# Kernel tuning notes

Hardware: AMD Instinct MI355X
Metric: run time of the kernel (lower is better)

## Reference

```python
import jax, jax.numpy as jnp
import numpy as np

GROUPS = 32
EPS = 1e-5


def group_norm(x, gamma, beta):
    B, C, D, H, W = x.shape
    xr = x.reshape(B, GROUPS, C // GROUPS, D, H, W)
    mean = xr.mean(axis=(2, 3, 4, 5), keepdims=True)
    var = xr.var(axis=(2, 3, 4, 5), keepdims=True)
    xn = (xr - mean) * jax.lax.rsqrt(var + EPS)
    xn = xn.reshape(B, C, D, H, W)
    return xn * gamma[None, :, None, None, None] + beta[None, :, None, None, None]


def conv1x1(h, w, b):
    # 1x1x1 Conv3d == channel matmul. w: [O, C], b: [O]
    return jnp.einsum('oc,bcdhw->bodhw', w, h) + b[None, :, None, None, None]


def setup_inputs() -> dict:
    key = jax.random.key(0)
    ks = jax.random.split(key, 10)
    B, C, D, H, W = 2, 128, 16, 16, 16
    x = jax.random.normal(ks[0], (B, C, D, H, W), dtype=jnp.float32)
    gn_w = jnp.ones((C,), dtype=jnp.float32)
    gn_b = jnp.zeros((C,), dtype=jnp.float32)
    # xavier_uniform for [C, C, 1, 1, 1] conv: fan_in = fan_out = C
    lim = float(np.sqrt(6.0 / (C + C)))
    wq = jax.random.uniform(ks[1], (C, C), jnp.float32, -lim, lim)
    wk = jax.random.uniform(ks[2], (C, C), jnp.float32, -lim, lim)
    wv = jax.random.uniform(ks[3], (C, C), jnp.float32, -lim, lim)
    wp = jax.random.uniform(ks[4], (C, C), jnp.float32, -lim, lim) * 1e-05
    bq = jnp.zeros((C,), jnp.float32)
    bk = jnp.zeros((C,), jnp.float32)
    bv = jnp.zeros((C,), jnp.float32)
    bp = jnp.zeros((C,), jnp.float32)
    return {"x": x, "gn_w": gn_w, "gn_b": gn_b, "wq": wq, "bq": bq,
            "wk": wk, "bk": bk, "wv": wv, "bv": bv, "wp": wp, "bp": bp}


def reference(x, gn_w, gn_b, wq, bq, wk, bk, wv, bv, wp, bp):
    B, C, D, H, W = x.shape
    N = D * H * W
    h = group_norm(x, gn_w, gn_b)
    q = conv1x1(h, wq, bq)
    k = conv1x1(h, wk, bk)
    v = conv1x1(h, wv, bv)
    q = q.transpose(0, 2, 3, 4, 1).reshape(B, N, C)   # [B, N, C]
    k = k.reshape(B, C, N)                            # [B, C, N]
    v = v.transpose(0, 2, 3, 4, 1).reshape(B, N, C)   # [B, N, C]
    w = jnp.einsum('bnc,bcm->bnm', q, k) * (C ** -0.5)  # [B, N, N]
    w = jax.nn.softmax(w, axis=-1)
    h = jnp.einsum('bnm,bmc->bnc', w, v)              # [B, N, C]
    h = h.reshape(B, D, H, W, C).transpose(0, 4, 1, 2, 3)
    h = conv1x1(h, wp, bp)
    return x + h
```

## Files before the change

kernel.cpp:

```cpp
#include <hip/hip_runtime.h>
#include <math.h>

#define CC 128
#define NN 4096
#define BB 2
#define NGROUPS 32
#define CPG 4
#define GSIZE (CPG*NN)
#define KSPLIT 8

typedef __attribute__((ext_vector_type(8))) __bf16 bf16x8;
typedef __attribute__((ext_vector_type(4))) float floatx4;

__device__ __forceinline__ unsigned short f2bf(float f) {
  union { float f; unsigned u; } v; v.f = f;
  unsigned r = v.u + 0x7fff + ((v.u >> 16) & 1);
  return (unsigned short)(r >> 16);
}
__device__ __forceinline__ float bf2f(unsigned short u) {
  return __uint_as_float(((unsigned)u) << 16);
}


__device__ __forceinline__ void stage_tile(const unsigned short* __restrict__ gtile,
                                           unsigned short* ltile, int w, int lane) {
  #pragma unroll
  for (int j = 0; j < 4; j++) {
    int off = (w*4 + j) * 512;
    __builtin_amdgcn_global_load_lds(
        (const __attribute__((address_space(1))) unsigned int*)(gtile + off + lane*8),
        (__attribute__((address_space(3))) unsigned int*)(ltile + off),
        16, 0, 0);
  }
}

__global__ void gn_stats_kernel(const float* __restrict__ x, float2* __restrict__ stats,
                                const float* __restrict__ wq, const float* __restrict__ wk,
                                const float* __restrict__ wv, const float* __restrict__ wp,
                                unsigned short* __restrict__ wqb, unsigned short* __restrict__ wkb,
                                unsigned short* __restrict__ wvb, unsigned short* __restrict__ wpb) {
  int t = threadIdx.x;
  if (blockIdx.x < 256) {
    int bid = blockIdx.x;
    const float4* base = (const float4*)(x + (size_t)bid * 4096);
    float4 v = base[t];
    float s  = v.x + v.y + v.z + v.w;
    float ss = v.x*v.x + v.y*v.y + v.z*v.z + v.w*v.w;
    #pragma unroll
    for (int off = 1; off < 64; off <<= 1) {
      s  += __shfl_xor(s, off);
      ss += __shfl_xor(ss, off);
    }
    __shared__ float sred[4], ssred[4];
    if ((t & 63) == 0) { sred[t >> 6] = s; ssred[t >> 6] = ss; }
    __syncthreads();
    if (t == 0)
      stats[bid] = make_float2(sred[0]+sred[1]+sred[2]+sred[3],
                               ssred[0]+ssred[1]+ssred[2]+ssred[3]);
  } else {
    const float sc = 0.08838834764831845f;
    int i = (blockIdx.x - 256) * 256 + t;
    int id = i >> 12, local = i & 4095;
    const float* src = id==0 ? wq : id==1 ? wk : id==2 ? wv : wp;
    unsigned short* dst = id==0 ? wqb : id==1 ? wkb : id==2 ? wvb : wpb;
    float s = (id == 0) ? sc : 1.0f;
    float4 v = ((const float4*)src)[local];
    unsigned p0 = (unsigned)f2bf(v.x*s) | ((unsigned)f2bf(v.y*s) << 16);
    unsigned p1 = (unsigned)f2bf(v.z*s) | ((unsigned)f2bf(v.w*s) << 16);
    ((uint2*)dst)[local] = make_uint2(p0, p1);
  }
}

__global__ __launch_bounds__(256, 2) void qkv_kernel(
    const float* __restrict__ x, const float2* __restrict__ stats,
    const float* __restrict__ gamma, const float* __restrict__ beta,
    const unsigned short* __restrict__ wqb, const unsigned short* __restrict__ wkb,
    const unsigned short* __restrict__ wvb,
    const float* __restrict__ bq, const float* __restrict__ bk, const float* __restrict__ bv,
    unsigned short* __restrict__ q, unsigned short* __restrict__ k, unsigned short* __restrict__ v) {
  int z = blockIdx.z, b = blockIdx.y, n0 = blockIdx.x * 32;
  const unsigned short* wsel = z==0 ? wqb : z==1 ? wkb : wvb;
  const float* bias          = z==0 ? bq  : z==1 ? bk  : bv;
  float bscale               = z==0 ? 0.08838834764831845f : 1.0f;
  unsigned short* outp       = z==0 ? q   : z==1 ? k   : v;
  __shared__ unsigned short hs[32][130];
  __shared__ unsigned short vs[32][136];
  __shared__ float gm[NGROUPS], gr[NGROUPS], aa[CC], ab[CC];
  int t = threadIdx.x;
  if (t < NGROUPS) {
    float su = 0.f, ssq = 0.f;
    #pragma unroll
    for (int j = 0; j < 4; j++) {
      float2 p = stats[(b*NGROUPS + t)*4 + j];
      su += p.x; ssq += p.y;
    }
    float mean = su * (1.0f/GSIZE);
    float var  = ssq * (1.0f/GSIZE) - mean*mean;
    gm[t] = mean;
    gr[t] = rsqrtf(var + 1e-5f);
  }
  __syncthreads();
  if (t < CC) {
    int g = t >> 2;
    float a = gr[g] * gamma[t];
    aa[t] = a;
    ab[t] = beta[t] - gm[g] * a;
  }
  __syncthreads();
  #pragma unroll
  for (int j = 0; j < 16; j++) {
    int idx = j*256 + t;
    int c = idx >> 5, n = idx & 31;
    float xv = x[((size_t)b*CC + c)*NN + n0 + n];
    hs[n][c] = f2bf(aa[c]*xv + ab[c]);
  }
  __syncthreads();
  int w = t >> 6, lane = t & 63, quad = lane >> 4, c = lane & 15;
  int o0 = w * 32;
  floatx4 acc[2][2];
  #pragma unroll
  for (int rt = 0; rt < 2; rt++)
    #pragma unroll
    for (int ct = 0; ct < 2; ct++) acc[rt][ct] = (floatx4){0.f,0.f,0.f,0.f};
  #pragma unroll
  for (int ks = 0; ks < 4; ks++) {
    bf16x8 af[2];
    af[0] = *(const bf16x8*)&hs[c     ][ks*32 + quad*8];
    af[1] = *(const bf16x8*)&hs[16 + c][ks*32 + quad*8];
    #pragma unroll
    for (int ct = 0; ct < 2; ct++) {
      bf16x8 bfr = *(const bf16x8*)(wsel + (size_t)(o0 + ct*16 + c)*CC + ks*32 + quad*8);
      acc[0][ct] = __builtin_amdgcn_mfma_f32_16x16x32_bf16(af[0], bfr, acc[0][ct], 0, 0, 0);
      acc[1][ct] = __builtin_amdgcn_mfma_f32_16x16x32_bf16(af[1], bfr, acc[1][ct], 0, 0, 0);
    }
  }
  if (z < 2) {
    size_t base = (size_t)b*NN*CC + ((size_t)(n0 >> 4))*2048 + w*512;
    #pragma unroll
    for (int ct = 0; ct < 2; ct++) {
      float bi = bias[o0 + ct*16 + c] * bscale;
      #pragma unroll
      for (int rt = 0; rt < 2; rt++)
        #pragma unroll
        for (int r = 0; r < 4; r++)
          outp[base + rt*2048 + (quad*4 + r)*32 + ct*16 + c] = f2bf(acc[rt][ct][r] + bi);
    }
  } else {
    #pragma unroll
    for (int ct = 0; ct < 2; ct++) {
      float bi = bias[o0 + ct*16 + c];
      #pragma unroll
      for (int rt = 0; rt < 2; rt++)
        #pragma unroll
        for (int r = 0; r < 4; r++)
          vs[rt*16 + quad*4 + r][o0 + ct*16 + c] = f2bf(acc[rt][ct][r] + bi);
    }
    __syncthreads();
    int ct = t >> 5;
    int rem = t & 31;
    int c16 = rem >> 1;
    int m0 = (rem & 1) * 16;
    int ch = ct*16 + c16;
    unsigned pk[8];
    #pragma unroll
    for (int j2 = 0; j2 < 8; j2++) {
      unsigned lo = vs[m0 + j2*2    ][ch];
      unsigned hi = vs[m0 + j2*2 + 1][ch];
      pk[j2] = lo | (hi << 16);
    }
    uint4* dst = (uint4*)(outp + (size_t)b*NN*CC + ((size_t)(n0 >> 5))*4096 + ct*512 + c16*32 + m0);
    dst[0] = make_uint4(pk[0], pk[1], pk[2], pk[3]);
    dst[1] = make_uint4(pk[4], pk[5], pk[6], pk[7]);
  }
}

__global__ __launch_bounds__(256, 2) void attn_kernel(
    const unsigned short* __restrict__ qm,
    const unsigned short* __restrict__ km,
    const unsigned short* __restrict__ vm,
    unsigned short* __restrict__ Opart,
    float* __restrict__ lpart) {
  int b    = blockIdx.z;
  int kh   = blockIdx.y;
  int t    = threadIdx.x;
  int w    = t >> 6, lane = t & 63, quad = lane >> 4, c = lane & 15;

  __shared__ unsigned short Kbuf[8192];
  __shared__ unsigned short Vbuf[8192];
  __shared__ unsigned short Pl[4][32][72];

  int fragoff = c*32 + quad*8;

  bf16x8 qa[2][4];
  const unsigned short* qbase = qm + (size_t)b*NN*CC + ((size_t)(blockIdx.x*8 + w*2))*2048;
  #pragma unroll
  for (int rt = 0; rt < 2; rt++)
    #pragma unroll
    for (int ks = 0; ks < 4; ks++)
      qa[rt][ks] = *(const bf16x8*)(qbase + rt*2048 + ks*512 + fragoff);

  floatx4 O[2][8];
  #pragma unroll
  for (int rt = 0; rt < 2; rt++)
    #pragma unroll
    for (int ct = 0; ct < 8; ct++) O[rt][ct] = (floatx4){0.f,0.f,0.f,0.f};
  float lsum[2][4];
  #pragma unroll
  for (int rt = 0; rt < 2; rt++)
    #pragma unroll
    for (int r = 0; r < 4; r++) lsum[rt][r] = 0.f;

  const unsigned short* kt0 = km + (size_t)b*NN*CC + (size_t)kh*32*2048;
  const unsigned short* vt0 = vm + (size_t)b*NN*CC + (size_t)kh*16*4096;

  const int ITERS = NN/KSPLIT/64;

  stage_tile(kt0, Kbuf, w, lane);
  stage_tile(vt0, Vbuf, w, lane);
  __syncthreads();

  for (int it = 0; it < ITERS; it++) {
    floatx4 S[2][4];
    #pragma unroll
    for (int rt = 0; rt < 2; rt++)
      #pragma unroll
      for (int ct = 0; ct < 4; ct++) S[rt][ct] = (floatx4){0.f,0.f,0.f,0.f};
    #pragma unroll
    for (int ks = 0; ks < 4; ks++) {
      #pragma unroll
      for (int ct = 0; ct < 4; ct++) {
        bf16x8 kf = *(const bf16x8*)&Kbuf[ct*2048 + ks*512 + fragoff];
        S[0][ct] = __builtin_amdgcn_mfma_f32_16x16x32_bf16(qa[0][ks], kf, S[0][ct], 0, 0, 0);
        S[1][ct] = __builtin_amdgcn_mfma_f32_16x16x32_bf16(qa[1][ks], kf, S[1][ct], 0, 0, 0);
      }
    }
    #pragma unroll
    for (int rt = 0; rt < 2; rt++) {
      #pragma unroll
      for (int ct = 0; ct < 4; ct++) {
        float e0 = __expf(S[rt][ct][0]);
        float e1 = __expf(S[rt][ct][1]);
        float e2 = __expf(S[rt][ct][2]);
        float e3 = __expf(S[rt][ct][3]);
        lsum[rt][0] += e0; lsum[rt][1] += e1;
        lsum[rt][2] += e2; lsum[rt][3] += e3;
        bool odd = (c & 1);
        float s01 = odd ? e0 : e1;
        float g01 = __shfl_xor(s01, 1);
        unsigned lo0 = __float_as_uint(odd ? g01 : e0);
        unsigned hi0 = __float_as_uint(odd ? e1 : g01);
        unsigned p0 = (hi0 & 0xffff0000u) | (lo0 >> 16);
        float s23 = odd ? e2 : e3;
        float g23 = __shfl_xor(s23, 1);
        unsigned lo1 = __float_as_uint(odd ? g23 : e2);
        unsigned hi1 = __float_as_uint(odd ? e3 : g23);
        unsigned p1 = (hi1 & 0xffff0000u) | (lo1 >> 16);
        int colpair = ct*16 + (c & ~1);
        int rowA = rt*16 + quad*4 + (odd ? 1 : 0);
        int rowB = rt*16 + quad*4 + (odd ? 3 : 2);
        *(unsigned*)&Pl[w][rowA][colpair] = p0;
        *(unsigned*)&Pl[w][rowB][colpair] = p1;
      }
    }
    __syncthreads();
    if (it+1 < ITERS) stage_tile(kt0 + (size_t)(it+1)*8192, Kbuf, w, lane);
    #pragma unroll
    for (int ks2 = 0; ks2 < 2; ks2++) {
      bf16x8 pa0 = *(const bf16x8*)(&Pl[w][c     ][ks2*32 + quad*8]);
      bf16x8 pa1 = *(const bf16x8*)(&Pl[w][16 + c][ks2*32 + quad*8]);
      #pragma unroll
      for (int ct = 0; ct < 8; ct++) {
        bf16x8 vf = *(const bf16x8*)&Vbuf[ks2*4096 + ct*512 + fragoff];
        O[0][ct] = __builtin_amdgcn_mfma_f32_16x16x32_bf16(pa0, vf, O[0][ct], 0, 0, 0);
        O[1][ct] = __builtin_amdgcn_mfma_f32_16x16x32_bf16(pa1, vf, O[1][ct], 0, 0, 0);
      }
    }
    __syncthreads();
    if (it+1 < ITERS) stage_tile(vt0 + (size_t)(it+1)*8192, Vbuf, w, lane);
  }

  size_t nbase = (size_t)(kh*BB + b)*NN + blockIdx.x*128 + w*32;
  #pragma unroll
  for (int rt = 0; rt < 2; rt++)
    #pragma unroll
    for (int r = 0; r < 4; r++) {
      float vsum = lsum[rt][r];
      vsum += __shfl_xor(vsum, 1);
      vsum += __shfl_xor(vsum, 2);
      vsum += __shfl_xor(vsum, 4);
      vsum += __shfl_xor(vsum, 8);
      if (c == 0) lpart[nbase + rt*16 + quad*4 + r] = vsum;
    }
  #pragma unroll
  for (int rt = 0; rt < 2; rt++)
    #pragma unroll
    for (int ct = 0; ct < 8; ct++)
      #pragma unroll
      for (int r = 0; r < 4; r++)
        Opart[(nbase + rt*16 + quad*4 + r)*CC + ct*16 + c] = f2bf(O[rt][ct][r]);
}

__global__ __launch_bounds__(256, 2) void combine_kernel(
    const unsigned short* __restrict__ Opart, const float* __restrict__ lpart,
    const unsigned short* __restrict__ wpb, const float* __restrict__ bp,
    const float* __restrict__ x, float* __restrict__ out) {
  int b = blockIdx.y, n0 = blockIdx.x * 32;
  int t = threadIdx.x;
  __shared__ unsigned short hs[32][130];
  __shared__ float ps[32][132];
  __shared__ float linv[32];
  if (t < 32) {
    float l = 0.f;
    #pragma unroll
    for (int kh = 0; kh < KSPLIT; kh++)
      l += lpart[((size_t)(kh*BB + b))*NN + n0 + t];
    linv[t] = 1.f / l;
  }
  __syncthreads();
  {
    int n = t >> 3, ch0 = (t & 7) * 16;
    float acc[16];
    #pragma unroll
    for (int j = 0; j < 16; j++) acc[j] = 0.f;
    #pragma unroll
    for (int kh = 0; kh < KSPLIT; kh++) {
      const uint4* src = (const uint4*)(Opart + ((size_t)(kh*BB + b)*NN + n0 + n)*CC + ch0);
      uint4 a = src[0], bv = src[1];
      unsigned uu[8] = {a.x, a.y, a.z, a.w, bv.x, bv.y, bv.z, bv.w};
      #pragma unroll
      for (int j = 0; j < 8; j++) {
        acc[j*2    ] += bf2f((unsigned short)(uu[j] & 0xffff));
        acc[j*2 + 1] += bf2f((unsigned short)(uu[j] >> 16));
      }
    }
    float li = linv[n];
    #pragma unroll
    for (int j = 0; j < 16; j++) hs[n][ch0 + j] = f2bf(acc[j] * li);
  }
  __syncthreads();
  int w = t >> 6, lane = t & 63, quad = lane >> 4, c = lane & 15;
  int o0 = w * 32;
  floatx4 acc[2][2];
  #pragma unroll
  for (int rt = 0; rt < 2; rt++)
    #pragma unroll
    for (int ct = 0; ct < 2; ct++) acc[rt][ct] = (floatx4){0.f,0.f,0.f,0.f};
  #pragma unroll
  for (int ks = 0; ks < 4; ks++) {
    bf16x8 af[2];
    af[0] = *(const bf16x8*)&hs[c     ][ks*32 + quad*8];
    af[1] = *(const bf16x8*)&hs[16 + c][ks*32 + quad*8];
    #pragma unroll
    for (int ct = 0; ct < 2; ct++) {
      bf16x8 bfr = *(const bf16x8*)(wpb + (size_t)(o0 + ct*16 + c)*CC + ks*32 + quad*8);
      acc[0][ct] = __builtin_amdgcn_mfma_f32_16x16x32_bf16(af[0], bfr, acc[0][ct], 0, 0, 0);
      acc[1][ct] = __builtin_amdgcn_mfma_f32_16x16x32_bf16(af[1], bfr, acc[1][ct], 0, 0, 0);
    }
  }
  #pragma unroll
  for (int rt = 0; rt < 2; rt++)
    #pragma unroll
    for (int ct = 0; ct < 2; ct++)
      #pragma unroll
      for (int r = 0; r < 4; r++)
        ps[rt*16 + quad*4 + r][o0 + ct*16 + c] = acc[rt][ct][r];
  __syncthreads();
  int o = t >> 1, nh = (t & 1) * 16;
  float bi = bp[o];
  const float* xr = x + ((size_t)b*CC + o)*NN + n0 + nh;
  float* orow = out + ((size_t)b*CC + o)*NN + n0 + nh;
  #pragma unroll
  for (int j4 = 0; j4 < 4; j4++) {
    float4 xv = ((const float4*)xr)[j4];
    float4 ov;
    ov.x = xv.x + ps[nh + j4*4 + 0][o] + bi;
    ov.y = xv.y + ps[nh + j4*4 + 1][o] + bi;
    ov.z = xv.z + ps[nh + j4*4 + 2][o] + bi;
    ov.w = xv.w + ps[nh + j4*4 + 3][o] + bi;
    ((float4*)orow)[j4] = ov;
  }
}

extern "C" void kernel_launch(void* const* d_in, const int* in_sizes, int n_in,
                              void* d_out, int out_size, void* d_ws, size_t ws_size,
                              hipStream_t stream) {
  const float* x    = (const float*)d_in[0];
  const float* gn_w = (const float*)d_in[1];
  const float* gn_b = (const float*)d_in[2];
  const float* wq   = (const float*)d_in[3];
  const float* bq   = (const float*)d_in[4];
  const float* wk   = (const float*)d_in[5];
  const float* bk   = (const float*)d_in[6];
  const float* wv   = (const float*)d_in[7];
  const float* bv   = (const float*)d_in[8];
  const float* wp   = (const float*)d_in[9];
  const float* bp   = (const float*)d_in[10];
  float* out = (float*)d_out;

  char* ws = (char*)d_ws;
  float2*         stats = (float2*)(ws);
  unsigned short* wqb   = (unsigned short*)(ws + 8192);
  unsigned short* wkb   = (unsigned short*)(ws + 8192 + 32768);
  unsigned short* wvb   = (unsigned short*)(ws + 8192 + 65536);
  unsigned short* wpb   = (unsigned short*)(ws + 8192 + 98304);
  unsigned short* qb    = (unsigned short*)(ws + 262144);
  unsigned short* kb    = (unsigned short*)(ws + 262144 + 2097152);
  unsigned short* vb    = (unsigned short*)(ws + 262144 + 2*2097152);
  unsigned short* Opart = (unsigned short*)(ws + 6553600);
  float*          lpart = (float*)(ws + 6553600 + 16777216);

  gn_stats_kernel<<<dim3(320), 256, 0, stream>>>(x, stats, wq, wk, wv, wp,
                                                 wqb, wkb, wvb, wpb);
  qkv_kernel     <<<dim3(NN/32, BB, 3), 256, 0, stream>>>(x, stats, gn_w, gn_b,
                                                          wqb, wkb, wvb, bq, bk, bv,
                                                          qb, kb, vb);
  attn_kernel    <<<dim3(NN/128, KSPLIT, BB), 256, 0, stream>>>(qb, kb, vb, Opart, lpart);
  combine_kernel <<<dim3(NN/32, BB), 256, 0, stream>>>(Opart, lpart, wpb, bp, x, out);
}
```

Measured before the change: 120.7 us.

## Halve attention query rows per block and vectorize GroupNorm input loads

The attention kernel now gives each wave 16 query rows instead of 32, so each block covers 64 queries and the grid doubles to NN/64 blocks. This spreads work over more blocks on a many-CU GPU and cuts accumulator register pressure. In exchange, each K/V tile staged into shared memory is reused by half as many queries, so global K/V traffic doubles. Separately, the qkv kernel now reads x as float4 instead of scalar floats.

After: 125.1 us. 3.7% more time.

```diff
diff --git a/kernel.cpp b/kernel.cpp
--- a/kernel.cpp
+++ b/kernel.cpp
@@ -108,11 +108,15 @@
   }
   __syncthreads();
   #pragma unroll
-  for (int j = 0; j < 16; j++) {
+  for (int j = 0; j < 4; j++) {
     int idx = j*256 + t;
-    int c = idx >> 5, n = idx & 31;
-    float xv = x[((size_t)b*CC + c)*NN + n0 + n];
-    hs[n][c] = f2bf(aa[c]*xv + ab[c]);
+    int c = idx >> 3, n4 = idx & 7;
+    float4 xv = *(const float4*)(x + ((size_t)b*CC + c)*NN + n0 + n4*4);
+    float a = aa[c], bc = ab[c];
+    hs[n4*4+0][c] = f2bf(a*xv.x + bc);
+    hs[n4*4+1][c] = f2bf(a*xv.y + bc);
+    hs[n4*4+2][c] = f2bf(a*xv.z + bc);
+    hs[n4*4+3][c] = f2bf(a*xv.w + bc);
   }
   __syncthreads();
   int w = t >> 6, lane = t & 63, quad = lane >> 4, c = lane & 15;
@@ -187,28 +191,22 @@
 
   __shared__ unsigned short Kbuf[8192];
   __shared__ unsigned short Vbuf[8192];
-  __shared__ unsigned short Pl[4][32][72];
+  __shared__ unsigned short Pl[4][16][72];
 
   int fragoff = c*32 + quad*8;
 
-  bf16x8 qa[2][4];
-  const unsigned short* qbase = qm + (size_t)b*NN*CC + ((size_t)(blockIdx.x*8 + w*2))*2048;
-  #pragma unroll
-  for (int rt = 0; rt < 2; rt++)
-    #pragma unroll
-    for (int ks = 0; ks < 4; ks++)
-      qa[rt][ks] = *(const bf16x8*)(qbase + rt*2048 + ks*512 + fragoff);
-
-  floatx4 O[2][8];
-  #pragma unroll
-  for (int rt = 0; rt < 2; rt++)
-    #pragma unroll
-    for (int ct = 0; ct < 8; ct++) O[rt][ct] = (floatx4){0.f,0.f,0.f,0.f};
-  float lsum[2][4];
-  #pragma unroll
-  for (int rt = 0; rt < 2; rt++)
-    #pragma unroll
-    for (int r = 0; r < 4; r++) lsum[rt][r] = 0.f;
+  bf16x8 qa[4];
+  const unsigned short* qbase = qm + (size_t)b*NN*CC + ((size_t)(blockIdx.x*4 + w))*2048;
+  #pragma unroll
+  for (int ks = 0; ks < 4; ks++)
+    qa[ks] = *(const bf16x8*)(qbase + ks*512 + fragoff);
+
+  floatx4 O[8];
+  #pragma unroll
+  for (int ct = 0; ct < 8; ct++) O[ct] = (floatx4){0.f,0.f,0.f,0.f};
+  float lsum[4];
+  #pragma unroll
+  for (int r = 0; r < 4; r++) lsum[r] = 0.f;
 
   const unsigned short* kt0 = km + (size_t)b*NN*CC + (size_t)kh*32*2048;
   const unsigned short* vt0 = vm + (size_t)b*NN*CC + (size_t)kh*16*4096;
@@ -220,84 +218,72 @@
   __syncthreads();
 
   for (int it = 0; it < ITERS; it++) {
-    floatx4 S[2][4];
-    #pragma unroll
-    for (int rt = 0; rt < 2; rt++)
-      #pragma unroll
-      for (int ct = 0; ct < 4; ct++) S[rt][ct] = (floatx4){0.f,0.f,0.f,0.f};
+    floatx4 S[4];
+    #pragma unroll
+    for (int ct = 0; ct < 4; ct++) S[ct] = (floatx4){0.f,0.f,0.f,0.f};
     #pragma unroll
     for (int ks = 0; ks < 4; ks++) {
       #pragma unroll
       for (int ct = 0; ct < 4; ct++) {
         bf16x8 kf = *(const bf16x8*)&Kbuf[ct*2048 + ks*512 + fragoff];
-        S[0][ct] = __builtin_amdgcn_mfma_f32_16x16x32_bf16(qa[0][ks], kf, S[0][ct], 0, 0, 0);
-        S[1][ct] = __builtin_amdgcn_mfma_f32_16x16x32_bf16(qa[1][ks], kf, S[1][ct], 0, 0, 0);
+        S[ct] = __builtin_amdgcn_mfma_f32_16x16x32_bf16(qa[ks], kf, S[ct], 0, 0, 0);
       }
     }
     #pragma unroll
-    for (int rt = 0; rt < 2; rt++) {
-      #pragma unroll
-      for (int ct = 0; ct < 4; ct++) {
-        float e0 = __expf(S[rt][ct][0]);
-        float e1 = __expf(S[rt][ct][1]);
-        float e2 = __expf(S[rt][ct][2]);
-        float e3 = __expf(S[rt][ct][3]);
-        lsum[rt][0] += e0; lsum[rt][1] += e1;
-        lsum[rt][2] += e2; lsum[rt][3] += e3;
-        bool odd = (c & 1);
-        float s01 = odd ? e0 : e1;
-        float g01 = __shfl_xor(s01, 1);
-        unsigned lo0 = __float_as_uint(odd ? g01 : e0);
-        unsigned hi0 = __float_as_uint(odd ? e1 : g01);
-        unsigned p0 = (hi0 & 0xffff0000u) | (lo0 >> 16);
-        float s23 = odd ? e2 : e3;
-        float g23 = __shfl_xor(s23, 1);
-        unsigned lo1 = __float_as_uint(odd ? g23 : e2);
-        unsigned hi1 = __float_as_uint(odd ? e3 : g23);
-        unsigned p1 = (hi1 & 0xffff0000u) | (lo1 >> 16);
-        int colpair = ct*16 + (c & ~1);
-        int rowA = rt*16 + quad*4 + (odd ? 1 : 0);
-        int rowB = rt*16 + quad*4 + (odd ? 3 : 2);
-        *(unsigned*)&Pl[w][rowA][colpair] = p0;
-        *(unsigned*)&Pl[w][rowB][colpair] = p1;
-      }
+    for (int ct = 0; ct < 4; ct++) {
+      float e0 = __expf(S[ct][0]);
+      float e1 = __expf(S[ct][1]);
+      float e2 = __expf(S[ct][2]);
+      float e3 = __expf(S[ct][3]);
+      lsum[0] += e0; lsum[1] += e1;
+      lsum[2] += e2; lsum[3] += e3;
+      bool odd = (c & 1);
+      float s01 = odd ? e0 : e1;
+      float g01 = __shfl_xor(s01, 1);
+      unsigned lo0 = __float_as_uint(odd ? g01 : e0);
+      unsigned hi0 = __float_as_uint(odd ? e1 : g01);
+      unsigned p0 = (hi0 & 0xffff0000u) | (lo0 >> 16);
+      float s23 = odd ? e2 : e3;
+      float g23 = __shfl_xor(s23, 1);
+      unsigned lo1 = __float_as_uint(odd ? g23 : e2);
+      unsigned hi1 = __float_as_uint(odd ? e3 : g23);
+      unsigned p1 = (hi1 & 0xffff0000u) | (lo1 >> 16);
+      int colpair = ct*16 + (c & ~1);
+      int rowA = quad*4 + (odd ? 1 : 0);
+      int rowB = quad*4 + (odd ? 3 : 2);
+      *(unsigned*)&Pl[w][rowA][colpair] = p0;
+      *(unsigned*)&Pl[w][rowB][colpair] = p1;
     }
     __syncthreads();
     if (it+1 < ITERS) stage_tile(kt0 + (size_t)(it+1)*8192, Kbuf, w, lane);
     #pragma unroll
     for (int ks2 = 0; ks2 < 2; ks2++) {
-      bf16x8 pa0 = *(const bf16x8*)(&Pl[w][c     ][ks2*32 + quad*8]);
-      bf16x8 pa1 = *(const bf16x8*)(&Pl[w][16 + c][ks2*32 + quad*8]);
+      bf16x8 pa = *(const bf16x8*)(&Pl[w][c][ks2*32 + quad*8]);
       #pragma unroll
       for (int ct = 0; ct < 8; ct++) {
         bf16x8 vf = *(const bf16x8*)&Vbuf[ks2*4096 + ct*512 + fragoff];
-        O[0][ct] = __builtin_amdgcn_mfma_f32_16x16x32_bf16(pa0, vf, O[0][ct], 0, 0, 0);
-        O[1][ct] = __builtin_amdgcn_mfma_f32_16x16x32_bf16(pa1, vf, O[1][ct], 0, 0, 0);
+        O[ct] = __builtin_amdgcn_mfma_f32_16x16x32_bf16(pa, vf, O[ct], 0, 0, 0);
       }
     }
     __syncthreads();
     if (it+1 < ITERS) stage_tile(vt0 + (size_t)(it+1)*8192, Vbuf, w, lane);
   }
 
-  size_t nbase = (size_t)(kh*BB + b)*NN + blockIdx.x*128 + w*32;
-  #pragma unroll
-  for (int rt = 0; rt < 2; rt++)
-    #pragma unroll
-    for (int r = 0; r < 4; r++) {
-      float vsum = lsum[rt][r];
-      vsum += __shfl_xor(vsum, 1);
-      vsum += __shfl_xor(vsum, 2);
-      vsum += __shfl_xor(vsum, 4);
-      vsum += __shfl_xor(vsum, 8);
-      if (c == 0) lpart[nbase + rt*16 + quad*4 + r] = vsum;
-    }
-  #pragma unroll
-  for (int rt = 0; rt < 2; rt++)
-    #pragma unroll
-    for (int ct = 0; ct < 8; ct++)
-      #pragma unroll
-      for (int r = 0; r < 4; r++)
-        Opart[(nbase + rt*16 + quad*4 + r)*CC + ct*16 + c] = f2bf(O[rt][ct][r]);
+  size_t nbase = (size_t)(kh*BB + b)*NN + blockIdx.x*64 + w*16;
+  #pragma unroll
+  for (int r = 0; r < 4; r++) {
+    float vsum = lsum[r];
+    vsum += __shfl_xor(vsum, 1);
+    vsum += __shfl_xor(vsum, 2);
+    vsum += __shfl_xor(vsum, 4);
+    vsum += __shfl_xor(vsum, 8);
+    if (c == 0) lpart[nbase + quad*4 + r] = vsum;
+  }
+  #pragma unroll
+  for (int ct = 0; ct < 8; ct++)
+    #pragma unroll
+    for (int r = 0; r < 4; r++)
+      Opart[(nbase + quad*4 + r)*CC + ct*16 + c] = f2bf(O[ct][r]);
 }
 
 __global__ __launch_bounds__(256, 2) void combine_kernel(
@@ -414,6 +400,6 @@
   qkv_kernel     <<<dim3(NN/32, BB, 3), 256, 0, stream>>>(x, stats, gn_w, gn_b,
                                                           wqb, wkb, wvb, bq, bk, bv,
                                                           qb, kb, vb);
-  attn_kernel    <<<dim3(NN/128, KSPLIT, BB), 256, 0, stream>>>(qb, kb, vb, Opart, lpart);
+  attn_kernel    <<<dim3(NN/64, KSPLIT, BB), 256, 0, stream>>>(qb, kb, vb, Opart, lpart);
   combine_kernel <<<dim3(NN/32, BB), 256, 0, stream>>>(Opart, lpart, wpb, bp, x, out);
 }
```

## Fuse Q/K/V projections into one block and halve row tiles in qkv and combine

Applied to the files above, without the earlier changes.

The QKV kernel now computes Q, K and V together in each block instead of one projection per z-slice. This lets the GroupNorm-normalized input tile be loaded once and the A fragments be reused across all three weight matrices. The row tile shrinks from 32 to 16 positions in both the qkv and combine kernels, doubling the block count to 512 to improve occupancy across CUs. The x load is vectorized to float4. The trade-off is less weight reuse per block, and more blocks each redo the per-group stat reduction.

Result: no change. 120.7 us (-0.0%).

```diff
diff --git a/kernel.cpp b/kernel.cpp
--- a/kernel.cpp
+++ b/kernel.cpp
@@ -78,13 +78,9 @@
     const unsigned short* __restrict__ wvb,
     const float* __restrict__ bq, const float* __restrict__ bk, const float* __restrict__ bv,
     unsigned short* __restrict__ q, unsigned short* __restrict__ k, unsigned short* __restrict__ v) {
-  int z = blockIdx.z, b = blockIdx.y, n0 = blockIdx.x * 32;
-  const unsigned short* wsel = z==0 ? wqb : z==1 ? wkb : wvb;
-  const float* bias          = z==0 ? bq  : z==1 ? bk  : bv;
-  float bscale               = z==0 ? 0.08838834764831845f : 1.0f;
-  unsigned short* outp       = z==0 ? q   : z==1 ? k   : v;
-  __shared__ unsigned short hs[32][130];
-  __shared__ unsigned short vs[32][136];
+  int b = blockIdx.y, n0 = blockIdx.x * 16;
+  __shared__ unsigned short hs[16][130];
+  __shared__ unsigned short vs[16][136];
   __shared__ float gm[NGROUPS], gr[NGROUPS], aa[CC], ab[CC];
   int t = threadIdx.x;
   if (t < NGROUPS) {
@@ -108,69 +104,78 @@
   }
   __syncthreads();
   #pragma unroll
-  for (int j = 0; j < 16; j++) {
+  for (int j = 0; j < 2; j++) {
     int idx = j*256 + t;
-    int c = idx >> 5, n = idx & 31;
-    float xv = x[((size_t)b*CC + c)*NN + n0 + n];
-    hs[n][c] = f2bf(aa[c]*xv + ab[c]);
+    int c = idx >> 2, n4 = idx & 3;
+    float4 xv = *(const float4*)(x + ((size_t)b*CC + c)*NN + n0 + n4*4);
+    float a = aa[c], bc = ab[c];
+    hs[n4*4+0][c] = f2bf(a*xv.x + bc);
+    hs[n4*4+1][c] = f2bf(a*xv.y + bc);
+    hs[n4*4+2][c] = f2bf(a*xv.z + bc);
+    hs[n4*4+3][c] = f2bf(a*xv.w + bc);
   }
   __syncthreads();
   int w = t >> 6, lane = t & 63, quad = lane >> 4, c = lane & 15;
   int o0 = w * 32;
-  floatx4 acc[2][2];
-  #pragma unroll
-  for (int rt = 0; rt < 2; rt++)
-    #pragma unroll
-    for (int ct = 0; ct < 2; ct++) acc[rt][ct] = (floatx4){0.f,0.f,0.f,0.f};
+  bf16x8 af[4];
+  #pragma unroll
+  for (int ks = 0; ks < 4; ks++)
+    af[ks] = *(const bf16x8*)&hs[c][ks*32 + quad*8];
+  floatx4 aq[2], ak[2], av[2];
+  #pragma unroll
+  for (int ct = 0; ct < 2; ct++) {
+    aq[ct] = (floatx4){0.f,0.f,0.f,0.f};
+    ak[ct] = (floatx4){0.f,0.f,0.f,0.f};
+    av[ct] = (floatx4){0.f,0.f,0.f,0.f};
+  }
   #pragma unroll
   for (int ks = 0; ks < 4; ks++) {
-    bf16x8 af[2];
-    af[0] = *(const bf16x8*)&hs[c     ][ks*32 + quad*8];
-    af[1] = *(const bf16x8*)&hs[16 + c][ks*32 + quad*8];
     #pragma unroll
     for (int ct = 0; ct < 2; ct++) {
-      bf16x8 bfr = *(const bf16x8*)(wsel + (size_t)(o0 + ct*16 + c)*CC + ks*32 + quad*8);
-      acc[0][ct] = __builtin_amdgcn_mfma_f32_16x16x32_bf16(af[0], bfr, acc[0][ct], 0, 0, 0);
-      acc[1][ct] = __builtin_amdgcn_mfma_f32_16x16x32_bf16(af[1], bfr, acc[1][ct], 0, 0, 0);
-    }
-  }
-  if (z < 2) {
-    size_t base = (size_t)b*NN*CC + ((size_t)(n0 >> 4))*2048 + w*512;
+      size_t woff = (size_t)(o0 + ct*16 + c)*CC + ks*32 + quad*8;
+      bf16x8 bq8 = *(const bf16x8*)(wqb + woff);
+      bf16x8 bk8 = *(const bf16x8*)(wkb + woff);
+      bf16x8 bv8 = *(const bf16x8*)(wvb + woff);
+      aq[ct] = __builtin_amdgcn_mfma_f32_16x16x32_bf16(af[ks], bq8, aq[ct], 0, 0, 0);
+      ak[ct] = __builtin_amdgcn_mfma_f32_16x16x32_bf16(af[ks], bk8, ak[ct], 0, 0, 0);
+      av[ct] = __builtin_amdgcn_mfma_f32_16x16x32_bf16(af[ks], bv8, av[ct], 0, 0, 0);
+    }
+  }
+  {
+    const float sc = 0.08838834764831845f;
+    size_t base = (size_t)b*NN*CC + (size_t)blockIdx.x*2048 + w*512;
     #pragma unroll
     for (int ct = 0; ct < 2; ct++) {
-      float bi = bias[o0 + ct*16 + c] * bscale;
-      #pragma unroll
-      for (int rt = 0; rt < 2; rt++)
-        #pragma unroll
-        for (int r = 0; r < 4; r++)
-          outp[base + rt*2048 + (quad*4 + r)*32 + ct*16 + c] = f2bf(acc[rt][ct][r] + bi);
-    }
-  } else {
-    #pragma unroll
-    for (int ct = 0; ct < 2; ct++) {
-      float bi = bias[o0 + ct*16 + c];
-      #pragma unroll
-      for (int rt = 0; rt < 2; rt++)
-        #pragma unroll
-        for (int r = 0; r < 4; r++)
-          vs[rt*16 + quad*4 + r][o0 + ct*16 + c] = f2bf(acc[rt][ct][r] + bi);
-    }
-    __syncthreads();
-    int ct = t >> 5;
-    int rem = t & 31;
-    int c16 = rem >> 1;
-    int m0 = (rem & 1) * 16;
-    int ch = ct*16 + c16;
-    unsigned pk[8];
-    #pragma unroll
-    for (int j2 = 0; j2 < 8; j2++) {
-      unsigned lo = vs[m0 + j2*2    ][ch];
-      unsigned hi = vs[m0 + j2*2 + 1][ch];
-      pk[j2] = lo | (hi << 16);
-    }
-    uint4* dst = (uint4*)(outp + (size_t)b*NN*CC + ((size_t)(n0 >> 5))*4096 + ct*512 + c16*32 + m0);
-    dst[0] = make_uint4(pk[0], pk[1], pk[2], pk[3]);
-    dst[1] = make_uint4(pk[4], pk[5], pk[6], pk[7]);
+      float bqi = bq[o0 + ct*16 + c] * sc;
+      float bki = bk[o0 + ct*16 + c];
+      #pragma unroll
+      for (int r = 0; r < 4; r++) {
+        int idx = (quad*4 + r)*32 + ct*16 + c;
+        q[base + idx] = f2bf(aq[ct][r] + bqi);
+        k[base + idx] = f2bf(ak[ct][r] + bki);
+      }
+    }
+  }
+  #pragma unroll
+  for (int ct = 0; ct < 2; ct++) {
+    float bvi = bv[o0 + ct*16 + c];
+    #pragma unroll
+    for (int r = 0; r < 4; r++)
+      vs[quad*4 + r][o0 + ct*16 + c] = f2bf(av[ct][r] + bvi);
+  }
+  __syncthreads();
+  {
+    int ch = t >> 1, part = t & 1;
+    int mbase = (n0 & 16) + part*8;
+    unsigned pk[4];
+    #pragma unroll
+    for (int j = 0; j < 4; j++) {
+      unsigned lo = vs[part*8 + j*2    ][ch];
+      unsigned hi = vs[part*8 + j*2 + 1][ch];
+      pk[j] = lo | (hi << 16);
+    }
+    *(uint4*)(v + (size_t)b*NN*CC + ((size_t)(n0 >> 5))*4096 + (ch >> 4)*512
+              + (ch & 15)*32 + mbase) = make_uint4(pk[0], pk[1], pk[2], pk[3]);
   }
 }
 
@@ -304,12 +309,12 @@
     const unsigned short* __restrict__ Opart, const float* __restrict__ lpart,
     const unsigned short* __restrict__ wpb, const float* __restrict__ bp,
     const float* __restrict__ x, float* __restrict__ out) {
-  int b = blockIdx.y, n0 = blockIdx.x * 32;
+  int b = blockIdx.y, n0 = blockIdx.x * 16;
   int t = threadIdx.x;
-  __shared__ unsigned short hs[32][130];
-  __shared__ float ps[32][132];
-  __shared__ float linv[32];
-  if (t < 32) {
+  __shared__ unsigned short hs[16][130];
+  __shared__ float ps[16][132];
+  __shared__ float linv[16];
+  if (t < 16) {
     float l = 0.f;
     #pragma unroll
     for (int kh = 0; kh < KSPLIT; kh++)
@@ -318,59 +323,51 @@
   }
   __syncthreads();
   {
-    int n = t >> 3, ch0 = (t & 7) * 16;
-    float acc[16];
-    #pragma unroll
-    for (int j = 0; j < 16; j++) acc[j] = 0.f;
+    int n = t >> 4, ch0 = (t & 15) * 8;
+    float acc[8];
+    #pragma unroll
+    for (int j = 0; j < 8; j++) acc[j] = 0.f;
     #pragma unroll
     for (int kh = 0; kh < KSPLIT; kh++) {
-      const uint4* src = (const uint4*)(Opart + ((size_t)(kh*BB + b)*NN + n0 + n)*CC + ch0);
-      uint4 a = src[0], bv = src[1];
-      unsigned uu[8] = {a.x, a.y, a.z, a.w, bv.x, bv.y, bv.z, bv.w};
-      #pragma unroll
-      for (int j = 0; j < 8; j++) {
+      uint4 a = *(const uint4*)(Opart + ((size_t)(kh*BB + b)*NN + n0 + n)*CC + ch0);
+      unsigned uu[4] = {a.x, a.y, a.z, a.w};
+      #pragma unroll
+      for (int j = 0; j < 4; j++) {
         acc[j*2    ] += bf2f((unsigned short)(uu[j] & 0xffff));
         acc[j*2 + 1] += bf2f((unsigned short)(uu[j] >> 16));
       }
     }
     float li = linv[n];
     #pragma unroll
-    for (int j = 0; j < 16; j++) hs[n][ch0 + j] = f2bf(acc[j] * li);
+    for (int j = 0; j < 8; j++) hs[n][ch0 + j] = f2bf(acc[j] * li);
   }
   __syncthreads();
   int w = t >> 6, lane = t & 63, quad = lane >> 4, c = lane & 15;
   int o0 = w * 32;
-  floatx4 acc[2][2];
-  #pragma unroll
-  for (int rt = 0; rt < 2; rt++)
-    #pragma unroll
-    for (int ct = 0; ct < 2; ct++) acc[rt][ct] = (floatx4){0.f,0.f,0.f,0.f};
+  floatx4 acc[2];
+  #pragma unroll
+  for (int ct = 0; ct < 2; ct++) acc[ct] = (floatx4){0.f,0.f,0.f,0.f};
   #pragma unroll
   for (int ks = 0; ks < 4; ks++) {
-    bf16x8 af[2];
-    af[0] = *(const bf16x8*)&hs[c     ][ks*32 + quad*8];
-    af[1] = *(const bf16x8*)&hs[16 + c][ks*32 + quad*8];
+    bf16x8 af = *(const bf16x8*)&hs[c][ks*32 + quad*8];
     #pragma unroll
     for (int ct = 0; ct < 2; ct++) {
       bf16x8 bfr = *(const bf16x8*)(wpb + (size_t)(o0 + ct*16 + c)*CC + ks*32 + quad*8);
-      acc[0][ct] = __builtin_amdgcn_mfma_f32_16x16x32_bf16(af[0], bfr, acc[0][ct], 0, 0, 0);
-      acc[1][ct] = __builtin_amdgcn_mfma_f32_16x16x32_bf16(af[1], bfr, acc[1][ct], 0, 0, 0);
-    }
-  }
-  #pragma unroll
-  for (int rt = 0; rt < 2; rt++)
-    #pragma unroll
-    for (int ct = 0; ct < 2; ct++)
-      #pragma unroll
-      for (int r = 0; r < 4; r++)
-        ps[rt*16 + quad*4 + r][o0 + ct*16 + c] = acc[rt][ct][r];
-  __syncthreads();
-  int o = t >> 1, nh = (t & 1) * 16;
+      acc[ct] = __builtin_amdgcn_mfma_f32_16x16x32_bf16(af, bfr, acc[ct], 0, 0, 0);
+    }
+  }
+  #pragma unroll
+  for (int ct = 0; ct < 2; ct++)
+    #pragma unroll
+    for (int r = 0; r < 4; r++)
+      ps[quad*4 + r][o0 + ct*16 + c] = acc[ct][r];
+  __syncthreads();
+  int o = t >> 1, nh = (t & 1) * 8;
   float bi = bp[o];
   const float* xr = x + ((size_t)b*CC + o)*NN + n0 + nh;
   float* orow = out + ((size_t)b*CC + o)*NN + n0 + nh;
   #pragma unroll
-  for (int j4 = 0; j4 < 4; j4++) {
+  for (int j4 = 0; j4 < 2; j4++) {
     float4 xv = ((const float4*)xr)[j4];
     float4 ov;
     ov.x = xv.x + ps[nh + j4*4 + 0][o] + bi;
@@ -411,9 +408,9 @@
 
   gn_stats_kernel<<<dim3(320), 256, 0, stream>>>(x, stats, wq, wk, wv, wp,
                                                  wqb, wkb, wvb, wpb);
-  qkv_kernel     <<<dim3(NN/32, BB, 3), 256, 0, stream>>>(x, stats, gn_w, gn_b,
-                                                          wqb, wkb, wvb, bq, bk, bv,
-                                                          qb, kb, vb);
+  qkv_kernel     <<<dim3(NN/16, BB), 256, 0, stream>>>(x, stats, gn_w, gn_b,
+                                                       wqb, wkb, wvb, bq, bk, bv,
+                                                       qb, kb, vb);
   attn_kernel    <<<dim3(NN/128, KSPLIT, BB), 256, 0, stream>>>(qb, kb, vb, Opart, lpart);
-  combine_kernel <<<dim3(NN/32, BB), 256, 0, stream>>>(Opart, lpart, wpb, bp, x, out);
-}
+  combine_kernel <<<dim3(NN/16, BB), 256, 0, stream>>>(Opart, lpart, wpb, bp, x, out);
+}
```
